# Kernel tuning notes

Hardware: AMD Instinct MI355X
Metric: run time of the kernel (lower is better)

The kernel has to match this reference:

```python
import jax, jax.numpy as jnp
import numpy as np

DIM_IN = 512
DIM_OUT = 64


def setup_inputs() -> dict:
    key = jax.random.key(0)
    kx, kq, kk, kv = jax.random.split(key, 4)
    x = jax.random.normal(kx, (4, 4096, DIM_IN), dtype=jnp.float32)
    s = 1.0 / np.sqrt(DIM_IN)
    # torch nn.Linear stores weight as [out, in]; keep same convention
    Wq = jax.random.uniform(kq, (DIM_OUT, DIM_IN), jnp.float32, -s, s)
    Wk = jax.random.uniform(kk, (DIM_OUT, DIM_IN), jnp.float32, -s, s)
    Wv = jax.random.uniform(kv, (DIM_OUT, DIM_IN), jnp.float32, -s, s)
    return {"x": x, "Wq": Wq, "Wk": Wk, "Wv": Wv}


def reference(x, Wq, Wk, Wv):
    # q/k/v projections: [B,S,Din] @ [Din,Dout] -> [B,S,Dout]
    q = jnp.einsum("bsd,od->bso", x, Wq)
    k = jnp.einsum("bsd,od->bso", x, Wk)
    v = jnp.einsum("bsd,od->bso", x, Wv)
    scale = 1.0 / jnp.sqrt(jnp.asarray(q.shape[-1], q.dtype))
    scores = jnp.einsum("bqo,bko->bqk", q, k) * scale  # [B,S,S]
    weights = jax.nn.softmax(scores, axis=-1)
    out = jnp.einsum("bqk,bko->bqo", weights, v)  # [B,S,Dout]
    return out
```

## Files before the change

### kernel.cpp

```cpp
#include <hip/hip_runtime.h>
#include <hip/hip_bf16.h>

#define SEQ 4096
#define MTOT 16384

typedef float f32x4  __attribute__((ext_vector_type(4)));
typedef float f32x16 __attribute__((ext_vector_type(16)));
typedef _Float16 f16;
typedef _Float16 f16x4 __attribute__((ext_vector_type(4)));
typedef _Float16 f16x8 __attribute__((ext_vector_type(8)));
typedef unsigned int   u32;
typedef unsigned int   u32x2 __attribute__((ext_vector_type(2)));
typedef unsigned short u16;

static constexpr size_t QL_B   = 0;
static constexpr size_t KL_B   = 2u << 20;
static constexpr size_t VL_B   = 4u << 20;
static constexpr size_t WL_B   = 6u << 20;

__device__ __forceinline__ u16 h16(float v) { return __builtin_bit_cast(u16, (f16)v); }
__device__ __forceinline__ u32 pkrtz(float a, float b) {
  return __builtin_bit_cast(u32, __builtin_amdgcn_cvt_pkrtz(a, b));
}
__device__ __forceinline__ float ex2(float x) { return __builtin_amdgcn_exp2f(x); }
__device__ __forceinline__ void gl16(const u16* g, u16* l) {
  __builtin_amdgcn_global_load_lds((const __attribute__((address_space(1))) void*)g,
                                   (__attribute__((address_space(3))) void*)l, 16, 0, 0);
}

__global__ __launch_bounds__(256) void wconv_kernel(const float* __restrict__ Wq,
                                                    const float* __restrict__ Wk,
                                                    const float* __restrict__ Wv,
                                                    u16* __restrict__ wlin) {
  const float QSC = 0.18033688011112042f;
  int e = blockIdx.x * 256 + threadIdx.x;
  int flat = e * 4;
  int colg = flat >> 9;
  int k0   = flat & 511;
  int mat  = colg >> 6;
  const float* W = (mat == 0) ? Wq : (mat == 1 ? Wk : Wv);
  f32x4 v = *(const f32x4*)(W + (size_t)(colg & 63) * 512 + k0);
  if (mat == 0) v *= QSC;
  int s = colg >> 4, r16 = colg & 15;
  int step = k0 >> 5, g = (k0 & 31) >> 3, jb = k0 & 7;
  __attribute__((aligned(8))) u16 b[4];
#pragma unroll
  for (int j = 0; j < 4; ++j) b[j] = h16(v[j]);
  *(uint2*)(wlin + ((size_t)(s * 16 + step) * 64 + g * 16 + r16) * 8 + jb) = *(uint2*)b;
}

__global__ __launch_bounds__(256, 4) void proj_kernel(const float* __restrict__ x,
                                                      const u16* __restrict__ wlin,
                                                      u16* __restrict__ ws) {
  __shared__ __attribute__((aligned(16))) u16 xl[8192];
  float* scr = (float*)xl;

  const int tid  = threadIdx.x;
  const int blk  = blockIdx.x;
  const int lane = tid & 63;
  const int ng   = tid >> 6;
  const int r16  = lane & 15;
  const int g    = lane >> 4;
  const int m0   = blk * 16;

#pragma unroll
  for (int i = 0; i < 8; ++i) {
    int f = tid * 4 + i * 1024;
    int row = f >> 9, k0 = f & 511;
    f32x4 v = *(const f32x4*)(x + (size_t)m0 * 512 + f);
    __attribute__((aligned(8))) u16 b[4];
#pragma unroll
    for (int j = 0; j < 4; ++j) b[j] = h16(v[j]);
    int ln = ((k0 & 31) >> 3) * 16 + row;
    *(uint2*)(xl + ((size_t)(k0 >> 5) * 64 + ln) * 8 + (k0 & 7)) = *(uint2*)b;
  }
  __syncthreads();

  f32x4 acc[3];
#pragma unroll
  for (int s = 0; s < 3; ++s) acc[s] = (f32x4){0.f, 0.f, 0.f, 0.f};

  f16x8 wfA[3], wfB[3], xA, xB;
  auto loadW = [&](f16x8(&wf)[3], int step) {
#pragma unroll
    for (int s = 0; s < 3; ++s)
      wf[s] = *(const f16x8*)(wlin + ((size_t)((ng * 3 + s) * 16 + step) * 64 + lane) * 8);
  };
  auto loadX = [&](f16x8& xf, int step) {
    xf = *(const f16x8*)(xl + ((size_t)step * 64 + lane) * 8);
  };

  loadW(wfA, 0);
  loadX(xA, 0);
#pragma unroll 1
  for (int sp = 0; sp < 8; ++sp) {
    loadW(wfB, 2 * sp + 1);
    loadX(xB, 2 * sp + 1);
#pragma unroll
    for (int s = 0; s < 3; ++s)
      acc[s] = __builtin_amdgcn_mfma_f32_16x16x32_f16(xA, wfA[s], acc[s], 0, 0, 0);
    if (sp < 7) {
      loadW(wfA, 2 * sp + 2);
      loadX(xA, 2 * sp + 2);
    }
#pragma unroll
    for (int s = 0; s < 3; ++s)
      acc[s] = __builtin_amdgcn_mfma_f32_16x16x32_f16(xB, wfB[s], acc[s], 0, 0, 0);
  }
  __syncthreads();

#pragma unroll
  for (int s = 0; s < 3; ++s)
#pragma unroll
    for (int rr = 0; rr < 4; ++rr)
      scr[(g * 4 + rr) * 193 + ng * 48 + s * 16 + r16] = acc[s][rr];
  __syncthreads();

  u16* Ql = ws + (QL_B >> 1);
  u16* Kl = ws + (KL_B >> 1);
  u16* Vl = ws + (VL_B >> 1);
  const int batch = m0 >> 12;
  const int tile  = (m0 >> 5) & 127;
  const int half  = (m0 >> 4) & 1;

  {
    int t2 = tid & 127;
    int r  = t2 & 15, hh = (t2 >> 4) & 1, ch = t2 >> 5;
    int l31 = half * 16 + r;
    __attribute__((aligned(16))) u16 b[8];
    if (tid < 128) {
#pragma unroll
      for (int j = 0; j < 8; ++j) b[j] = h16(scr[r * 193 + 64 + ch * 16 + hh * 8 + j]);
      *(uint4*)(Kl + ((size_t)((batch * 128 + tile) * 4 + ch) * 64 + hh * 32 + l31) * 8) =
          *(uint4*)b;
    } else {
#pragma unroll
      for (int j = 0; j < 8; ++j) b[j] = h16(scr[r * 193 + ch * 16 + hh * 8 + j]);
      int qhalf = (m0 >> 5);
      *(uint4*)(Ql + ((size_t)(qhalf * 4 + ch) * 64 + hh * 32 + l31) * 8) = *(uint4*)b;
    }
  }
  {
    int z = tid & 1, l31 = (tid >> 1) & 31, hh = (tid >> 6) & 1, db = tid >> 7;
    int d = db * 32 + l31;
    __attribute__((aligned(8))) u16 b[4];
#pragma unroll
    for (int j = 0; j < 4; ++j) b[j] = h16(scr[(8 * z + 4 * hh + j) * 193 + 128 + d]);
    *(uint2*)(Vl + ((size_t)(((batch * 128 + tile) * 2 + db) * 2 + half) * 64 + hh * 32 + l31) *
                       8 + z * 4) = *(uint2*)b;
  }
}

__global__ __launch_bounds__(512, 2) void attn_kernel(const u16* __restrict__ ws,
                                                      float* __restrict__ out) {
  __shared__ __attribute__((aligned(16))) u16 kb[8][2][2048];

  const int tid  = threadIdx.x;
  const int w    = tid >> 6;
  const int lane = tid & 63;
  const int l31  = lane & 31;
  const int h    = lane >> 5;
  const int qg   = w >> 2;
  const int kq   = w & 3;
  const int bx   = blockIdx.x;
  const int qb   = (bx & 7) * 32 + (bx >> 3);
  const int bb   = qb >> 6;

  const u16* Ql = ws + (QL_B >> 1);
  const u16* Kl = ws + (KL_B >> 1);
  const u16* Vl = ws + (VL_B >> 1);

  f16x8 qf[4];
#pragma unroll
  for (int ch = 0; ch < 4; ++ch)
    qf[ch] = *(const f16x8*)(Ql + ((size_t)((qb * 2 + qg) * 4 + ch) * 64 + lane) * 8);

  f32x16 oacc[2];
#pragma unroll
  for (int db = 0; db < 2; ++db)
#pragma unroll
    for (int r = 0; r < 16; ++r) oacc[db][r] = 0.f;
  float mrun = -INFINITY, lrun = 0.f;
  const float RTHR = 11.0f;

  const int t0 = bb * 128 + kq * 32;
  u16* b0 = &kb[w][0][0];
  u16* b1 = &kb[w][1][0];

  auto stageK = [&](u16* buf, int t) {
    const u16* ks = Kl + (size_t)t * 2048;
#pragma unroll
    for (int c = 0; c < 4; ++c) gl16(ks + c * 512 + lane * 8, buf + c * 512);
  };
  f16x8 v0[2][2], v1[2][2];
  auto loadV = [&](f16x8(&vv)[2][2], int t) {
#pragma unroll
    for (int db = 0; db < 2; ++db)
#pragma unroll
      for (int pp = 0; pp < 2; ++pp)
        vv[db][pp] = *(const f16x8*)(Vl + (size_t)t * 2048 + ((db * 2 + pp) * 64 + lane) * 8);
  };

  auto body = [&](u16* cb, u16* nb, f16x8(&vc)[2][2], f16x8(&vn)[2][2], int t, bool last) {
    if (!last) {
      stageK(nb, t + 1);
      loadV(vn, t + 1);
      asm volatile("s_waitcnt vmcnt(8)" ::: "memory");
    } else {
      asm volatile("s_waitcnt vmcnt(0)" ::: "memory");
    }
    __builtin_amdgcn_sched_barrier(0);

    f16x8 ka[4];
#pragma unroll
    for (int ch = 0; ch < 4; ++ch) ka[ch] = *(const f16x8*)(cb + (ch * 64 + lane) * 8);

    f32x16 sac;
#pragma unroll
    for (int r = 0; r < 16; ++r) sac[r] = 0.f;
#pragma unroll
    for (int ch = 0; ch < 4; ++ch)
      sac = __builtin_amdgcn_mfma_f32_32x32x16_f16(ka[ch], qf[ch], sac, 0, 0, 0);

    float t8[8];
#pragma unroll
    for (int r = 0; r < 8; ++r) t8[r] = fmaxf(sac[2 * r], sac[2 * r + 1]);
    float t4a = fmaxf(t8[0], t8[1]), t4b = fmaxf(t8[2], t8[3]);
    float t4c = fmaxf(t8[4], t8[5]), t4d = fmaxf(t8[6], t8[7]);
    float mt = fmaxf(fmaxf(t4a, t4b), fmaxf(t4c, t4d));
    if (__any(mt > mrun + RTHR)) {
      float mtw  = fmaxf(mt, __shfl_xor(mt, 32));
      float nm   = fmaxf(mrun, mtw);
      float corr = ex2(mrun - nm);
      lrun *= corr;
      mrun = nm;
#pragma unroll
      for (int db = 0; db < 2; ++db)
#pragma unroll
        for (int r = 0; r < 16; ++r) oacc[db][r] *= corr;
    }
#pragma unroll
    for (int r = 0; r < 16; ++r) sac[r] = ex2(sac[r] - mrun);
    float s4[4];
#pragma unroll
    for (int r = 0; r < 4; ++r)
      s4[r] = (sac[4 * r] + sac[4 * r + 1]) + (sac[4 * r + 2] + sac[4 * r + 3]);
    lrun += (s4[0] + s4[1]) + (s4[2] + s4[3]);

    f16x4 pb[4];
#pragma unroll
    for (int c = 0; c < 4; ++c) {
      u32x2 pk;
      pk[0] = pkrtz(sac[4 * c + 0], sac[4 * c + 1]);
      pk[1] = pkrtz(sac[4 * c + 2], sac[4 * c + 3]);
      pb[c] = __builtin_bit_cast(f16x4, pk);
    }

#pragma unroll
    for (int db = 0; db < 2; ++db)
#pragma unroll
      for (int pp = 0; pp < 2; ++pp) {
        f16x4 vlo = __builtin_shufflevector(vc[db][pp], vc[db][pp], 0, 1, 2, 3);
        f16x4 vhi = __builtin_shufflevector(vc[db][pp], vc[db][pp], 4, 5, 6, 7);
        oacc[db] = __builtin_amdgcn_mfma_f32_32x32x8f16(vlo, pb[2 * pp], oacc[db], 0, 0, 0);
        oacc[db] = __builtin_amdgcn_mfma_f32_32x32x8f16(vhi, pb[2 * pp + 1], oacc[db], 0, 0, 0);
      }
  };

  stageK(b0, t0);
  loadV(v0, t0);
#pragma unroll 1
  for (int p = 0; p < 16; ++p) {
    body(b0, b1, v0, v1, t0 + 2 * p, false);
    body(b1, b0, v1, v0, t0 + 2 * p + 1, p == 15);
  }

  lrun += __shfl_xor(lrun, 32);

  __syncthreads();
  float* po  = (float*)&kb[0][0][0];
  float* mls = (float*)((char*)&kb[0][0][0] + 36864);
  if (h == 0) {
    mls[(w * 32 + l31) * 2 + 0] = mrun;
    mls[(w * 32 + l31) * 2 + 1] = lrun;
  }
  __syncthreads();

#pragma unroll 1
  for (int g = 0; g < 2; ++g) {
    if (qg == g) {
      float mg = -INFINITY;
#pragma unroll
      for (int k2 = 0; k2 < 4; ++k2) mg = fmaxf(mg, mls[((g * 4 + k2) * 32 + l31) * 2]);
      float wgt = ex2(mrun - mg);
#pragma unroll
      for (int db = 0; db < 2; ++db)
#pragma unroll
        for (int gg = 0; gg < 4; ++gg) {
          f32x4 v = {oacc[db][4 * gg + 0] * wgt, oacc[db][4 * gg + 1] * wgt,
                     oacc[db][4 * gg + 2] * wgt, oacc[db][4 * gg + 3] * wgt};
          *(f32x4*)(po + (size_t)(kq * 32 + l31) * 68 + db * 32 + 8 * gg + 4 * h) = v;
        }
    }
    __syncthreads();
    {
      int q = tid >> 4, c4 = (tid & 15) * 4;
      float m2 = -INFINITY;
#pragma unroll
      for (int k2 = 0; k2 < 4; ++k2) m2 = fmaxf(m2, mls[((g * 4 + k2) * 32 + q) * 2]);
      float l2 = 0.f;
#pragma unroll
      for (int k2 = 0; k2 < 4; ++k2)
        l2 += mls[((g * 4 + k2) * 32 + q) * 2 + 1] * ex2(mls[((g * 4 + k2) * 32 + q) * 2] - m2);
      f32x4 s = (f32x4){0.f, 0.f, 0.f, 0.f};
#pragma unroll
      for (int k2 = 0; k2 < 4; ++k2) s += *(const f32x4*)(po + (size_t)(k2 * 32 + q) * 68 + c4);
      s *= (1.f / l2);
      *(f32x4*)(out + (size_t)(qb * 64 + g * 32 + q) * 64 + c4) = s;
    }
    __syncthreads();
  }
}

extern "C" void kernel_launch(void* const* d_in, const int* in_sizes, int n_in,
                              void* d_out, int out_size, void* d_ws, size_t ws_size,
                              hipStream_t stream) {
  const float* x  = (const float*)d_in[0];
  const float* Wq = (const float*)d_in[1];
  const float* Wk = (const float*)d_in[2];
  const float* Wv = (const float*)d_in[3];
  u16* ws = (u16*)d_ws;
  (void)in_sizes; (void)n_in; (void)out_size; (void)ws_size;

  wconv_kernel<<<96, 256, 0, stream>>>(Wq, Wk, Wv, ws + (WL_B >> 1));
  proj_kernel<<<1024, 256, 0, stream>>>(x, ws + (WL_B >> 1), ws);
  attn_kernel<<<256, 512, 0, stream>>>(ws, (float*)d_out);
}
```

Measured before the change: 54.79 us.

## Have each wave process both query groups over half the key tiles

Each wave now computes scores for both 32-row query groups against its own K tile, so every K and V tile it loads feeds two MFMA chains. Each wave covers 16 key tiles instead of 32, and the block's 64 queries are split across 8 key partitions. V is loaded within the iteration instead of double-buffered in registers, with waitcnts placed to overlap it with the softmax. MFMA sections get raised wave priority, and the final combine uses LDS atomicAdd across 8 waves in place of the two-pass staged reduction. This aims to cut K/V load traffic per FLOP, at the cost of more registers, less V prefetch slack and LDS atomic contention in the epilogue.

```diff
diff --git a/kernel.cpp b/kernel.cpp
--- a/kernel.cpp
+++ b/kernel.cpp
@@ -160,30 +160,34 @@
   const int lane = tid & 63;
   const int l31  = lane & 31;
   const int h    = lane >> 5;
-  const int qg   = w >> 2;
-  const int kq   = w & 3;
   const int bx   = blockIdx.x;
   const int qb   = (bx & 7) * 32 + (bx >> 3);
   const int bb   = qb >> 6;
+  const int q0   = qb * 64;
 
   const u16* Ql = ws + (QL_B >> 1);
   const u16* Kl = ws + (KL_B >> 1);
   const u16* Vl = ws + (VL_B >> 1);
 
-  f16x8 qf[4];
-#pragma unroll
-  for (int ch = 0; ch < 4; ++ch)
-    qf[ch] = *(const f16x8*)(Ql + ((size_t)((qb * 2 + qg) * 4 + ch) * 64 + lane) * 8);
-
-  f32x16 oacc[2];
-#pragma unroll
-  for (int db = 0; db < 2; ++db)
-#pragma unroll
-    for (int r = 0; r < 16; ++r) oacc[db][r] = 0.f;
-  float mrun = -INFINITY, lrun = 0.f;
+  f16x8 qf[2][4];
+#pragma unroll
+  for (int qg = 0; qg < 2; ++qg)
+#pragma unroll
+    for (int ch = 0; ch < 4; ++ch)
+      qf[qg][ch] = *(const f16x8*)(Ql + ((size_t)((qb * 2 + qg) * 4 + ch) * 64 + lane) * 8);
+
+  f32x16 oacc[2][2];
+#pragma unroll
+  for (int qg = 0; qg < 2; ++qg)
+#pragma unroll
+    for (int db = 0; db < 2; ++db)
+#pragma unroll
+      for (int r = 0; r < 16; ++r) oacc[qg][db][r] = 0.f;
+  float mrun[2] = {-INFINITY, -INFINITY};
+  float lrun[2] = {0.f, 0.f};
   const float RTHR = 11.0f;
 
-  const int t0 = bb * 128 + kq * 32;
+  const int t0 = bb * 128 + w * 16;
   u16* b0 = &kb[w][0][0];
   u16* b1 = &kb[w][1][0];
 
@@ -192,133 +196,154 @@
 #pragma unroll
     for (int c = 0; c < 4; ++c) gl16(ks + c * 512 + lane * 8, buf + c * 512);
   };
-  f16x8 v0[2][2], v1[2][2];
-  auto loadV = [&](f16x8(&vv)[2][2], int t) {
+
+  auto body = [&](u16* cb, u16* nb, int t, bool last) {
+    f16x8 vv[2][2];
 #pragma unroll
     for (int db = 0; db < 2; ++db)
 #pragma unroll
       for (int pp = 0; pp < 2; ++pp)
         vv[db][pp] = *(const f16x8*)(Vl + (size_t)t * 2048 + ((db * 2 + pp) * 64 + lane) * 8);
-  };
-
-  auto body = [&](u16* cb, u16* nb, f16x8(&vc)[2][2], f16x8(&vn)[2][2], int t, bool last) {
     if (!last) {
       stageK(nb, t + 1);
-      loadV(vn, t + 1);
       asm volatile("s_waitcnt vmcnt(8)" ::: "memory");
     } else {
+      asm volatile("s_waitcnt vmcnt(4)" ::: "memory");
+    }
+    __builtin_amdgcn_sched_barrier(0);
+
+    f16x8 ka[4];
+#pragma unroll
+    for (int ch = 0; ch < 4; ++ch) ka[ch] = *(const f16x8*)(cb + (ch * 64 + lane) * 8);
+
+    f32x16 sac[2];
+#pragma unroll
+    for (int qg = 0; qg < 2; ++qg)
+#pragma unroll
+      for (int r = 0; r < 16; ++r) sac[qg][r] = 0.f;
+    __builtin_amdgcn_s_setprio(1);
+#pragma unroll
+    for (int qg = 0; qg < 2; ++qg)
+#pragma unroll
+      for (int ch = 0; ch < 4; ++ch)
+        sac[qg] = __builtin_amdgcn_mfma_f32_32x32x16_f16(ka[ch], qf[qg][ch], sac[qg], 0, 0, 0);
+    __builtin_amdgcn_s_setprio(0);
+
+    f16x4 pb[2][4];
+#pragma unroll
+    for (int qg = 0; qg < 2; ++qg) {
+      float t8[8];
+#pragma unroll
+      for (int r = 0; r < 8; ++r) t8[r] = fmaxf(sac[qg][2 * r], sac[qg][2 * r + 1]);
+      float t4a = fmaxf(t8[0], t8[1]), t4b = fmaxf(t8[2], t8[3]);
+      float t4c = fmaxf(t8[4], t8[5]), t4d = fmaxf(t8[6], t8[7]);
+      float mt = fmaxf(fmaxf(t4a, t4b), fmaxf(t4c, t4d));
+      if (__any(mt > mrun[qg] + RTHR)) {
+        float mtw  = fmaxf(mt, __shfl_xor(mt, 32));
+        float nm   = fmaxf(mrun[qg], mtw);
+        float corr = ex2(mrun[qg] - nm);
+        lrun[qg] *= corr;
+        mrun[qg] = nm;
+#pragma unroll
+        for (int db = 0; db < 2; ++db)
+#pragma unroll
+          for (int r = 0; r < 16; ++r) oacc[qg][db][r] *= corr;
+      }
+#pragma unroll
+      for (int r = 0; r < 16; ++r) sac[qg][r] = ex2(sac[qg][r] - mrun[qg]);
+      float s4[4];
+#pragma unroll
+      for (int r = 0; r < 4; ++r)
+        s4[r] = (sac[qg][4 * r] + sac[qg][4 * r + 1]) + (sac[qg][4 * r + 2] + sac[qg][4 * r + 3]);
+      lrun[qg] += (s4[0] + s4[1]) + (s4[2] + s4[3]);
+#pragma unroll
+      for (int c = 0; c < 4; ++c) {
+        u32x2 pk;
+        pk[0] = pkrtz(sac[qg][4 * c + 0], sac[qg][4 * c + 1]);
+        pk[1] = pkrtz(sac[qg][4 * c + 2], sac[qg][4 * c + 3]);
+        pb[qg][c] = __builtin_bit_cast(f16x4, pk);
+      }
+    }
+
+    if (!last) {
+      asm volatile("s_waitcnt vmcnt(4)" ::: "memory");
+    } else {
       asm volatile("s_waitcnt vmcnt(0)" ::: "memory");
     }
     __builtin_amdgcn_sched_barrier(0);
 
-    f16x8 ka[4];
-#pragma unroll
-    for (int ch = 0; ch < 4; ++ch) ka[ch] = *(const f16x8*)(cb + (ch * 64 + lane) * 8);
-
-    f32x16 sac;
-#pragma unroll
-    for (int r = 0; r < 16; ++r) sac[r] = 0.f;
-#pragma unroll
-    for (int ch = 0; ch < 4; ++ch)
-      sac = __builtin_amdgcn_mfma_f32_32x32x16_f16(ka[ch], qf[ch], sac, 0, 0, 0);
-
-    float t8[8];
-#pragma unroll
-    for (int r = 0; r < 8; ++r) t8[r] = fmaxf(sac[2 * r], sac[2 * r + 1]);
-    float t4a = fmaxf(t8[0], t8[1]), t4b = fmaxf(t8[2], t8[3]);
-    float t4c = fmaxf(t8[4], t8[5]), t4d = fmaxf(t8[6], t8[7]);
-    float mt = fmaxf(fmaxf(t4a, t4b), fmaxf(t4c, t4d));
-    if (__any(mt > mrun + RTHR)) {
-      float mtw  = fmaxf(mt, __shfl_xor(mt, 32));
-      float nm   = fmaxf(mrun, mtw);
-      float corr = ex2(mrun - nm);
-      lrun *= corr;
-      mrun = nm;
-#pragma unroll
-      for (int db = 0; db < 2; ++db)
-#pragma unroll
-        for (int r = 0; r < 16; ++r) oacc[db][r] *= corr;
-    }
-#pragma unroll
-    for (int r = 0; r < 16; ++r) sac[r] = ex2(sac[r] - mrun);
-    float s4[4];
-#pragma unroll
-    for (int r = 0; r < 4; ++r)
-      s4[r] = (sac[4 * r] + sac[4 * r + 1]) + (sac[4 * r + 2] + sac[4 * r + 3]);
-    lrun += (s4[0] + s4[1]) + (s4[2] + s4[3]);
-
-    f16x4 pb[4];
-#pragma unroll
-    for (int c = 0; c < 4; ++c) {
-      u32x2 pk;
-      pk[0] = pkrtz(sac[4 * c + 0], sac[4 * c + 1]);
-      pk[1] = pkrtz(sac[4 * c + 2], sac[4 * c + 3]);
-      pb[c] = __builtin_bit_cast(f16x4, pk);
-    }
-
+    __builtin_amdgcn_s_setprio(1);
 #pragma unroll
     for (int db = 0; db < 2; ++db)
 #pragma unroll
       for (int pp = 0; pp < 2; ++pp) {
-        f16x4 vlo = __builtin_shufflevector(vc[db][pp], vc[db][pp], 0, 1, 2, 3);
-        f16x4 vhi = __builtin_shufflevector(vc[db][pp], vc[db][pp], 4, 5, 6, 7);
-        oacc[db] = __builtin_amdgcn_mfma_f32_32x32x8f16(vlo, pb[2 * pp], oacc[db], 0, 0, 0);
-        oacc[db] = __builtin_amdgcn_mfma_f32_32x32x8f16(vhi, pb[2 * pp + 1], oacc[db], 0, 0, 0);
+        f16x4 vlo = __builtin_shufflevector(vv[db][pp], vv[db][pp], 0, 1, 2, 3);
+        f16x4 vhi = __builtin_shufflevector(vv[db][pp], vv[db][pp], 4, 5, 6, 7);
+#pragma unroll
+        for (int qg = 0; qg < 2; ++qg) {
+          oacc[qg][db] =
+              __builtin_amdgcn_mfma_f32_32x32x8f16(vlo, pb[qg][2 * pp], oacc[qg][db], 0, 0, 0);
+          oacc[qg][db] = __builtin_amdgcn_mfma_f32_32x32x8f16(vhi, pb[qg][2 * pp + 1],
+                                                              oacc[qg][db], 0, 0, 0);
+        }
       }
+    __builtin_amdgcn_s_setprio(0);
   };
 
   stageK(b0, t0);
-  loadV(v0, t0);
 #pragma unroll 1
-  for (int p = 0; p < 16; ++p) {
-    body(b0, b1, v0, v1, t0 + 2 * p, false);
-    body(b1, b0, v1, v0, t0 + 2 * p + 1, p == 15);
-  }
-
-  lrun += __shfl_xor(lrun, 32);
+  for (int p = 0; p < 8; ++p) {
+    body(b0, b1, t0 + 2 * p, false);
+    body(b1, b0, t0 + 2 * p + 1, p == 7);
+  }
+
+#pragma unroll
+  for (int qg = 0; qg < 2; ++qg) lrun[qg] += __shfl_xor(lrun[qg], 32);
 
   __syncthreads();
   float* po  = (float*)&kb[0][0][0];
-  float* mls = (float*)((char*)&kb[0][0][0] + 36864);
+  float* mls = (float*)((char*)&kb[0][0][0] + 20480);
   if (h == 0) {
-    mls[(w * 32 + l31) * 2 + 0] = mrun;
-    mls[(w * 32 + l31) * 2 + 1] = lrun;
-  }
-  __syncthreads();
-
-#pragma unroll 1
-  for (int g = 0; g < 2; ++g) {
-    if (qg == g) {
-      float mg = -INFINITY;
-#pragma unroll
-      for (int k2 = 0; k2 < 4; ++k2) mg = fmaxf(mg, mls[((g * 4 + k2) * 32 + l31) * 2]);
-      float wgt = ex2(mrun - mg);
-#pragma unroll
-      for (int db = 0; db < 2; ++db)
-#pragma unroll
-        for (int gg = 0; gg < 4; ++gg) {
-          f32x4 v = {oacc[db][4 * gg + 0] * wgt, oacc[db][4 * gg + 1] * wgt,
-                     oacc[db][4 * gg + 2] * wgt, oacc[db][4 * gg + 3] * wgt};
-          *(f32x4*)(po + (size_t)(kq * 32 + l31) * 68 + db * 32 + 8 * gg + 4 * h) = v;
-        }
-    }
-    __syncthreads();
-    {
-      int q = tid >> 4, c4 = (tid & 15) * 4;
-      float m2 = -INFINITY;
-#pragma unroll
-      for (int k2 = 0; k2 < 4; ++k2) m2 = fmaxf(m2, mls[((g * 4 + k2) * 32 + q) * 2]);
-      float l2 = 0.f;
-#pragma unroll
-      for (int k2 = 0; k2 < 4; ++k2)
-        l2 += mls[((g * 4 + k2) * 32 + q) * 2 + 1] * ex2(mls[((g * 4 + k2) * 32 + q) * 2] - m2);
-      f32x4 s = (f32x4){0.f, 0.f, 0.f, 0.f};
-#pragma unroll
-      for (int k2 = 0; k2 < 4; ++k2) s += *(const f32x4*)(po + (size_t)(k2 * 32 + q) * 68 + c4);
-      s *= (1.f / l2);
-      *(f32x4*)(out + (size_t)(qb * 64 + g * 32 + q) * 64 + c4) = s;
-    }
-    __syncthreads();
+#pragma unroll
+    for (int qg = 0; qg < 2; ++qg) {
+      mls[((w * 2 + qg) * 32 + l31) * 2 + 0] = mrun[qg];
+      mls[((w * 2 + qg) * 32 + l31) * 2 + 1] = lrun[qg];
+    }
+  }
+  for (int idx = tid; idx < 64 * 68; idx += 512) po[idx] = 0.f;
+  __syncthreads();
+
+#pragma unroll
+  for (int qg = 0; qg < 2; ++qg) {
+    float mg = -INFINITY;
+#pragma unroll
+    for (int ww = 0; ww < 8; ++ww) mg = fmaxf(mg, mls[((ww * 2 + qg) * 32 + l31) * 2]);
+    float wgt = ex2(mrun[qg] - mg);
+#pragma unroll
+    for (int db = 0; db < 2; ++db)
+#pragma unroll
+      for (int r = 0; r < 16; ++r) {
+        int d = db * 32 + (r & 3) + 8 * (r >> 2) + 4 * h;
+        atomicAdd(&po[(qg * 32 + l31) * 68 + d], oacc[qg][db][r] * wgt);
+      }
+  }
+  __syncthreads();
+
+#pragma unroll
+  for (int i = 0; i < 2; ++i) {
+    int idx = tid + i * 512;
+    int q = idx >> 4, c4 = (idx & 15) * 4;
+    int qg2 = q >> 5, qr = q & 31;
+    float m2 = -INFINITY;
+#pragma unroll
+    for (int ww = 0; ww < 8; ++ww) m2 = fmaxf(m2, mls[((ww * 2 + qg2) * 32 + qr) * 2]);
+    float l2 = 0.f;
+#pragma unroll
+    for (int ww = 0; ww < 8; ++ww)
+      l2 += mls[((ww * 2 + qg2) * 32 + qr) * 2 + 1] * ex2(mls[((ww * 2 + qg2) * 32 + qr) * 2] - m2);
+    f32x4 s = *(const f32x4*)(po + (size_t)q * 68 + c4);
+    s *= (1.f / l2);
+    *(f32x4*)(out + (size_t)(q0 + q) * 64 + c4) = s;
   }
 }
 
```

Measured after the change: 92.04 us. 1.68x slower.
